# Performance work log

Measured on AMD Instinct MI355X. Metric: run time of the kernel, lower is better.

The kernel has to match this reference:

```python
import jax, jax.numpy as jnp
import numpy as np

INDEX_SHIFT = jnp.array([[0, 0], [-1, 0], [1, 0], [0, 1], [-1, 1], [1, 1], [0, -1], [-1, -1], [1, -1]], dtype=jnp.int32)
GRID = jnp.array([513, 513], dtype=jnp.int32)  # pseudo_image_dims + 1


def setup_inputs() -> dict:
    key = jax.random.key(0)
    k1, k2, k3, k4 = jax.random.split(key, 4)
    li_bev_coors = jax.random.randint(k1, (8192, 2), 0, 512, dtype=jnp.int32)
    ra_bev_coors = jax.random.randint(k2, (2048, 2), 0, 512, dtype=jnp.int32)
    ra_pts = jax.random.normal(k3, (2048, 5), dtype=jnp.float32)
    ra_voxel_coords = jax.random.randint(k4, (2048, 3), 0, 512, dtype=jnp.int32)
    return {"li_bev_coors": li_bev_coors, "ra_bev_coors": ra_bev_coors,
            "ra_pts": ra_pts, "ra_voxel_coords": ra_voxel_coords}


def _neighbour_coors(bev_grids):
    # [N,2] -> [N,9,2]: shift by 9-neighborhood, wrap by (grid_size+1)
    return (bev_grids[:, None, :] + INDEX_SHIFT[None, :, :]) % GRID


def _nearest_dy(neighbour_coor, dy_coor, dy_mask):
    # neighbour_coor: [N,9,2] int; dy_coor: [M,2] float; dy_mask: [M] bool
    n = neighbour_coor.shape[0]
    a = neighbour_coor.reshape(-1, 2).astype(jnp.float32)        # [N*9, 2]
    a2 = jnp.sum(a * a, axis=-1)                                  # [N*9]
    b2 = jnp.sum(dy_coor * dy_coor, axis=-1)                      # [M]
    # squared euclidean distances (exact: integer coordinates)
    d2 = a2[:, None] + b2[None, :] - 2.0 * (a @ dy_coor.T)        # [N*9, M]
    d2 = jnp.where(dy_mask[None, :], d2, jnp.inf)                 # mask non-dynamic voxels
    dmin = jnp.sqrt(jnp.maximum(jnp.min(d2, axis=-1), 0.0))       # min commutes with sqrt
    return (dmin * 0.01).reshape(n, 9)


def reference(li_bev_coors, ra_bev_coors, ra_pts, ra_voxel_coords):
    # dynamic-point selection: |velocity| > 0.1 (column 4)
    dy_mask = jnp.abs(ra_pts[:, 4]) > 0.1                         # [M]
    dy_coor = ra_voxel_coords[:, 1:].astype(jnp.float32)          # [M,2]
    # (uniquifying dy_coor does not change the min-distance; skip for jit shapes)
    li_nb = _neighbour_coors(li_bev_coors)                        # [N_li,9,2]
    ra_nb = _neighbour_coors(ra_bev_coors)                        # [N_ra,9,2]
    use = jnp.sum(dy_mask) > 1
    li_dis = jnp.where(use, _nearest_dy(li_nb, dy_coor, dy_mask), 0.0)
    ra_dis = jnp.where(use, _nearest_dy(ra_nb, dy_coor, dy_mask), 0.0)
    return (li_dis, ra_dis)
```

## Files before the change

kernel.cpp:

```cpp
#include <hip/hip_runtime.h>

#define BLOCK 256
#define SPLITS 16
#define QPT 8
#define PREPB 90
#define MAXC 136


__device__ __forceinline__ float2 pk_fma2(float2 a, float2 b, float2 c) {
    return make_float2(fmaf(a.x, b.x, c.x), fmaf(a.y, b.y, c.y));
}
__device__ __forceinline__ float2 pk_mul2(float2 a, float2 b) {
    return make_float2(a.x * b.x, a.y * b.y);
}

__global__ __launch_bounds__(BLOCK) void prep_kernel(
    const float* __restrict__ pts, int m,
    int* __restrict__ gate, int* __restrict__ out_bits, int total)
{
    __shared__ int s_cnt;
    const int tid = blockIdx.x * BLOCK + threadIdx.x;
    const int n4 = total >> 2;
    const int4 iv = make_int4(0x7F7F7F7F, 0x7F7F7F7F, 0x7F7F7F7F, 0x7F7F7F7F);
    int4* o4 = (int4*)out_bits;
    for (int i = tid; i < n4; i += PREPB * BLOCK) o4[i] = iv;

    if (blockIdx.x == 0) {
        if (threadIdx.x == 0) s_cnt = 0;
        __syncthreads();
        int nv = 0;
        for (int i = threadIdx.x; i < m; i += BLOCK)
            nv += (fabsf(pts[i * 5 + 4]) > 0.1f) ? 1 : 0;
        if (nv) atomicAdd(&s_cnt, nv);
        __syncthreads();
        if (threadIdx.x == 0) *gate = (s_cnt > 1) ? 1 : 0;
    }
}

__global__ __launch_bounds__(BLOCK) void main_kernel(
    const int* __restrict__ li_coors, int n_li,
    const int* __restrict__ ra_coors, int n_ra,
    const float* __restrict__ pts,
    const int* __restrict__ vox,
    int m, int cs, int csPad,
    const int* __restrict__ gate,
    int* __restrict__ out_bits, int total)
{
    __shared__ __align__(16) float sx[MAXC];
    __shared__ __align__(16) float sy[MAXC];

    const int g = *gate;

    const int li_total = n_li * 9;
    const int qbase = blockIdx.x * (BLOCK * QPT) + threadIdx.x;

    float n2x[QPT], n2y[QPT], q2[QPT], mn[QPT];
#pragma unroll
    for (int k = 0; k < QPT; ++k) {
        int q = qbase + k * BLOCK;
        float qx = 0.0f, qy = 0.0f;
        if (q < total) {
            const int shift_x[9] = {0,-1,1,0,-1,1,0,-1,1};
            const int shift_y[9] = {0, 0,0,1, 1,1,-1,-1,-1};
            int n, s;
            const int* src;
            if (q < li_total) { n = q / 9; s = q - n * 9; src = li_coors; }
            else { int r = q - li_total; n = r / 9; s = r - n * 9; src = ra_coors; }
            int cx = src[n * 2 + 0] + shift_x[s];
            int cy = src[n * 2 + 1] + shift_y[s];
            if (cx < 0) cx += 513;
            if (cy < 0) cy += 513;
            qx = (float)cx; qy = (float)cy;
        }
        n2x[k] = -2.0f * qx;
        n2y[k] = -2.0f * qy;
        q2[k]  = fmaf(qx, qx, qy * qy);
        mn[k]  = 3.4e38f;
    }

    const int base = blockIdx.y * cs;
    for (int i = threadIdx.x; i < csPad; i += BLOCK) {
        int gi = base + i;
        float x = 3.0e4f, y = 3.0e4f;
        if (i < cs && gi < m && fabsf(pts[gi * 5 + 4]) > 0.1f) {
            x = (float)vox[gi * 3 + 1];
            y = (float)vox[gi * 3 + 2];
        }
        sx[i] = x;
        sy[i] = y;
    }
    __syncthreads();

    const float4* __restrict__ X4 = (const float4*)sx;
    const float4* __restrict__ Y4 = (const float4*)sy;
    const int iters = csPad >> 2;
#pragma unroll 4
    for (int i = 0; i < iters; ++i) {
        float4 X = X4[i];
        float4 Y = Y4[i];
        float2 X01 = make_float2(X.x, X.y), X23 = make_float2(X.z, X.w);
        float2 Y01 = make_float2(Y.x, Y.y), Y23 = make_float2(Y.z, Y.w);
        float2 C01 = pk_fma2(X01, X01, pk_mul2(Y01, Y01));
        float2 C23 = pk_fma2(X23, X23, pk_mul2(Y23, Y23));
#pragma unroll
        for (int k = 0; k < QPT; ++k) {
            float2 nx = make_float2(n2x[k], n2x[k]);
            float2 ny = make_float2(n2y[k], n2y[k]);
            float2 T01 = pk_fma2(X01, nx, pk_fma2(Y01, ny, C01));
            float2 T23 = pk_fma2(X23, nx, pk_fma2(Y23, ny, C23));
            mn[k] = fminf(fminf(T01.x, T01.y), mn[k]);
            mn[k] = fminf(fminf(T23.x, T23.y), mn[k]);
        }
    }

#pragma unroll
    for (int k = 0; k < QPT; ++k) {
        int q = qbase + k * BLOCK;
        if (q < total) {
            float val = g ? sqrtf(q2[k] + mn[k]) * 0.01f : 0.0f;
            atomicMin(out_bits + q, __float_as_int(val));
        }
    }
}

extern "C" void kernel_launch(void* const* d_in, const int* in_sizes, int n_in,
                              void* d_out, int out_size, void* d_ws, size_t ws_size,
                              hipStream_t stream) {
    const int*   li  = (const int*)d_in[0];
    const int*   ra  = (const int*)d_in[1];
    const float* pts = (const float*)d_in[2];
    const int*   vox = (const int*)d_in[3];

    const int n_li = in_sizes[0] / 2;
    const int n_ra = in_sizes[1] / 2;
    const int m    = in_sizes[2] / 5;

    const int total = (n_li + n_ra) * 9;
    const int qblocks = (total + BLOCK * QPT - 1) / (BLOCK * QPT);

    const int cs    = (m + SPLITS - 1) / SPLITS;
    const int csPad = (cs + 3) & ~3;

    int* gate = (int*)d_ws;
    int* outb = (int*)d_out;

    prep_kernel<<<PREPB, BLOCK, 0, stream>>>(pts, m, gate, outb, total);
    main_kernel<<<dim3(qblocks, SPLITS), BLOCK, 0, stream>>>(
        li, n_li, ra, n_ra, pts, vox, m, cs, csPad, gate, outb, total);
}
```

Before: 79.06 us.

## Replace atomicMin output merge with workspace partials and a separate reduce kernel

When the workspace is large enough, each split block writes its partial squared minimum into a per-split workspace slice instead of doing atomicMin on the output. A new reduce kernel takes the min across the 16 splits, recomputes the dynamic-point gate per block, and writes the final sqrt-scaled distance. This drops the prep kernel's output initialisation and the atomics. In exchange it adds about 5.9 MB of workspace writes and reads, and every reduce block redundantly rescans the 2048 points for the gate count.

```diff
diff --git a/kernel.cpp b/kernel.cpp
--- a/kernel.cpp
+++ b/kernel.cpp
@@ -5,6 +5,7 @@
 #define QPT 8
 #define PREPB 90
 #define MAXC 136
+#define RQPT 4
 
 
 __device__ __forceinline__ float2 pk_fma2(float2 a, float2 b, float2 c) {
@@ -37,6 +38,7 @@
     }
 }
 
+template<bool WS_PATH>
 __global__ __launch_bounds__(BLOCK) void main_kernel(
     const int* __restrict__ li_coors, int n_li,
     const int* __restrict__ ra_coors, int n_ra,
@@ -44,12 +46,14 @@
     const int* __restrict__ vox,
     int m, int cs, int csPad,
     const int* __restrict__ gate,
+    float* __restrict__ ws,
     int* __restrict__ out_bits, int total)
 {
     __shared__ __align__(16) float sx[MAXC];
     __shared__ __align__(16) float sy[MAXC];
 
-    const int g = *gate;
+    int g = 1;
+    if (!WS_PATH) g = *gate;
 
     const int li_total = n_li * 9;
     const int qbase = blockIdx.x * (BLOCK * QPT) + threadIdx.x;
@@ -113,13 +117,59 @@
         }
     }
 
-#pragma unroll
-    for (int k = 0; k < QPT; ++k) {
+    if (WS_PATH) {
+        float* __restrict__ dst = ws + (size_t)blockIdx.y * (size_t)total;
+#pragma unroll
+        for (int k = 0; k < QPT; ++k) {
+            int q = qbase + k * BLOCK;
+            if (q < total) dst[q] = q2[k] + mn[k];
+        }
+    } else {
+#pragma unroll
+        for (int k = 0; k < QPT; ++k) {
+            int q = qbase + k * BLOCK;
+            if (q < total) {
+                float val = g ? sqrtf(q2[k] + mn[k]) * 0.01f : 0.0f;
+                atomicMin(out_bits + q, __float_as_int(val));
+            }
+        }
+    }
+}
+
+__global__ __launch_bounds__(BLOCK) void reduce_kernel(
+    const float* __restrict__ pts, int m,
+    const float* __restrict__ ws,
+    float* __restrict__ out, int total)
+{
+    __shared__ int s_cnt;
+    if (threadIdx.x == 0) s_cnt = 0;
+
+    const int qbase = blockIdx.x * (BLOCK * RQPT) + threadIdx.x;
+    float mnv[RQPT];
+#pragma unroll
+    for (int k = 0; k < RQPT; ++k) {
+        mnv[k] = 3.4e38f;
         int q = qbase + k * BLOCK;
         if (q < total) {
-            float val = g ? sqrtf(q2[k] + mn[k]) * 0.01f : 0.0f;
-            atomicMin(out_bits + q, __float_as_int(val));
-        }
+#pragma unroll
+            for (int s = 0; s < SPLITS; ++s)
+                mnv[k] = fminf(mnv[k], ws[(size_t)s * (size_t)total + q]);
+        }
+    }
+
+    __syncthreads();
+    int nv = 0;
+    for (int i = threadIdx.x; i < m; i += BLOCK)
+        nv += (fabsf(pts[i * 5 + 4]) > 0.1f) ? 1 : 0;
+    if (nv) atomicAdd(&s_cnt, nv);
+    __syncthreads();
+    const int g = (s_cnt > 1) ? 1 : 0;
+
+#pragma unroll
+    for (int k = 0; k < RQPT; ++k) {
+        int q = qbase + k * BLOCK;
+        if (q < total)
+            out[q] = g ? sqrtf(fmaxf(mnv[k], 0.0f)) * 0.01f : 0.0f;
     }
 }
 
@@ -141,10 +191,22 @@
     const int cs    = (m + SPLITS - 1) / SPLITS;
     const int csPad = (cs + 3) & ~3;
 
-    int* gate = (int*)d_ws;
-    int* outb = (int*)d_out;
-
-    prep_kernel<<<PREPB, BLOCK, 0, stream>>>(pts, m, gate, outb, total);
-    main_kernel<<<dim3(qblocks, SPLITS), BLOCK, 0, stream>>>(
-        li, n_li, ra, n_ra, pts, vox, m, cs, csPad, gate, outb, total);
-}
+    const size_t need = (size_t)SPLITS * (size_t)total * sizeof(float);
+
+    if (ws_size >= need) {
+        float* ws  = (float*)d_ws;
+        float* out = (float*)d_out;
+        main_kernel<true><<<dim3(qblocks, SPLITS), BLOCK, 0, stream>>>(
+            li, n_li, ra, n_ra, pts, vox, m, cs, csPad,
+            nullptr, ws, nullptr, total);
+        const int rblocks = (total + BLOCK * RQPT - 1) / (BLOCK * RQPT);
+        reduce_kernel<<<rblocks, BLOCK, 0, stream>>>(pts, m, ws, out, total);
+    } else {
+        int* gate = (int*)d_ws;
+        int* outb = (int*)d_out;
+        prep_kernel<<<PREPB, BLOCK, 0, stream>>>(pts, m, gate, outb, total);
+        main_kernel<false><<<dim3(qblocks, SPLITS), BLOCK, 0, stream>>>(
+            li, n_li, ra, n_ra, pts, vox, m, cs, csPad,
+            gate, nullptr, outb, total);
+    }
+}
```

Result: slower. 81.51 us (+3.1%).

## Fuse prep into main kernel with last-block split reduction via tickets

Applied to the files above, without the earlier changes.

The separate prep kernel, which initialised the output and computed the dynamic-point gate, is replaced with a hipMemsetAsync of a small counter region plus a single fused kernel. Each split block writes its partial minima to workspace and counts dynamic points with a wavefront ballot. The last block to arrive for each query tile, detected with an atomic ticket, reduces the partials and writes the final distances directly, replacing the per-element atomicMin. This removes one kernel launch and the atomics, but adds workspace traffic and a memset, and only runs when the workspace is large enough.

```diff
diff --git a/kernel.cpp b/kernel.cpp
--- a/kernel.cpp
+++ b/kernel.cpp
@@ -5,6 +5,8 @@
 #define QPT 8
 #define PREPB 90
 #define MAXC 136
+
+static_assert(MAXC <= BLOCK, "ballot-based gate count assumes <=1 staging iter/thread");
 
 
 __device__ __forceinline__ float2 pk_fma2(float2 a, float2 b, float2 c) {
@@ -37,19 +39,27 @@
     }
 }
 
+template<bool FUSED>
 __global__ __launch_bounds__(BLOCK) void main_kernel(
     const int* __restrict__ li_coors, int n_li,
     const int* __restrict__ ra_coors, int n_ra,
     const float* __restrict__ pts,
     const int* __restrict__ vox,
     int m, int cs, int csPad,
+    int* __restrict__ tickets,
+    int* __restrict__ gates,
+    float* __restrict__ part,
+    float* __restrict__ out,
     const int* __restrict__ gate,
-    int* __restrict__ out_bits, int total)
+    int* __restrict__ out_bits,
+    int total)
 {
     __shared__ __align__(16) float sx[MAXC];
     __shared__ __align__(16) float sy[MAXC];
-
-    const int g = *gate;
+    __shared__ int s_ret;
+
+    int g = 1;
+    if (!FUSED) g = *gate;
 
     const int li_total = n_li * 9;
     const int qbase = blockIdx.x * (BLOCK * QPT) + threadIdx.x;
@@ -79,15 +89,23 @@
     }
 
     const int base = blockIdx.y * cs;
+    bool dyn = false;
     for (int i = threadIdx.x; i < csPad; i += BLOCK) {
         int gi = base + i;
         float x = 3.0e4f, y = 3.0e4f;
         if (i < cs && gi < m && fabsf(pts[gi * 5 + 4]) > 0.1f) {
+            dyn = true;
             x = (float)vox[gi * 3 + 1];
             y = (float)vox[gi * 3 + 2];
         }
         sx[i] = x;
         sy[i] = y;
+    }
+
+    if (FUSED) {
+        unsigned long long b = __ballot(dyn);
+        if ((threadIdx.x & 63) == 0 && b)
+            atomicAdd(&gates[blockIdx.x], (int)__popcll(b));
     }
     __syncthreads();
 
@@ -113,12 +131,42 @@
         }
     }
 
-#pragma unroll
-    for (int k = 0; k < QPT; ++k) {
-        int q = qbase + k * BLOCK;
-        if (q < total) {
-            float val = g ? sqrtf(q2[k] + mn[k]) * 0.01f : 0.0f;
-            atomicMin(out_bits + q, __float_as_int(val));
+    if (FUSED) {
+        float* __restrict__ dst =
+            part + ((size_t)blockIdx.x * SPLITS + blockIdx.y) * (BLOCK * QPT);
+#pragma unroll
+        for (int k = 0; k < QPT; ++k)
+            dst[k * BLOCK + threadIdx.x] = q2[k] + mn[k];
+
+        __threadfence();
+        if (threadIdx.x == 0)
+            s_ret = atomicAdd(&tickets[blockIdx.x], 1);
+        __syncthreads();
+
+        if (s_ret == SPLITS - 1) {
+            __threadfence();
+            const int gg = gates[blockIdx.x];
+            const float* __restrict__ colp =
+                part + (size_t)blockIdx.x * SPLITS * (BLOCK * QPT);
+#pragma unroll
+            for (int k = 0; k < QPT; ++k) {
+                float v = q2[k] + mn[k];
+#pragma unroll 4
+                for (int y = 0; y < SPLITS; ++y)
+                    v = fminf(v, colp[y * (BLOCK * QPT) + k * BLOCK + threadIdx.x]);
+                int q = qbase + k * BLOCK;
+                if (q < total)
+                    out[q] = (gg > 1) ? sqrtf(fmaxf(v, 0.0f)) * 0.01f : 0.0f;
+            }
+        }
+    } else {
+#pragma unroll
+        for (int k = 0; k < QPT; ++k) {
+            int q = qbase + k * BLOCK;
+            if (q < total) {
+                float val = g ? sqrtf(q2[k] + mn[k]) * 0.01f : 0.0f;
+                atomicMin(out_bits + q, __float_as_int(val));
+            }
         }
     }
 }
@@ -141,10 +189,26 @@
     const int cs    = (m + SPLITS - 1) / SPLITS;
     const int csPad = (cs + 3) & ~3;
 
-    int* gate = (int*)d_ws;
-    int* outb = (int*)d_out;
-
-    prep_kernel<<<PREPB, BLOCK, 0, stream>>>(pts, m, gate, outb, total);
-    main_kernel<<<dim3(qblocks, SPLITS), BLOCK, 0, stream>>>(
-        li, n_li, ra, n_ra, pts, vox, m, cs, csPad, gate, outb, total);
-}
+    const size_t partOffF = 2048;
+    const size_t need =
+        (partOffF + (size_t)qblocks * SPLITS * (BLOCK * QPT)) * sizeof(float);
+
+    if (ws_size >= need && 2 * qblocks <= (int)partOffF && csPad <= MAXC) {
+        int*   tickets = (int*)d_ws;
+        int*   gates   = tickets + qblocks;
+        float* part    = (float*)d_ws + partOffF;
+        float* out     = (float*)d_out;
+
+        hipMemsetAsync(d_ws, 0, 2 * qblocks * sizeof(int), stream);
+        main_kernel<true><<<dim3(qblocks, SPLITS), BLOCK, 0, stream>>>(
+            li, n_li, ra, n_ra, pts, vox, m, cs, csPad,
+            tickets, gates, part, out, nullptr, nullptr, total);
+    } else {
+        int* gate = (int*)d_ws;
+        int* outb = (int*)d_out;
+        prep_kernel<<<PREPB, BLOCK, 0, stream>>>(pts, m, gate, outb, total);
+        main_kernel<false><<<dim3(qblocks, SPLITS), BLOCK, 0, stream>>>(
+            li, n_li, ra, n_ra, pts, vox, m, cs, csPad,
+            nullptr, nullptr, nullptr, nullptr, gate, outb, total);
+    }
+}
```

Result: slower. 170.6 us (+115.8%).

## Merge into single kernel with full dynamic-point set per block, no atomics

Applied to the files above, without the earlier changes.

Replaces the prep plus split-reduction design with one kernel. Each thread handles a single query, and each block stages up to 2048 candidate points (x, y and precomputed x²+y²) in shared memory. The gate count is computed inside every block, so the separate init kernel and the atomicMin output merge both go away. The cost is that every block reloads all candidates, and each thread carries one query instead of eight, which cuts register reuse per shared-memory load and adds three LDS reads per four candidates.

```diff
diff --git a/kernel.cpp b/kernel.cpp
--- a/kernel.cpp
+++ b/kernel.cpp
@@ -1,126 +1,99 @@
 #include <hip/hip_runtime.h>
 
-#define BLOCK 256
-#define SPLITS 16
-#define QPT 8
-#define PREPB 90
-#define MAXC 136
+#define BLOCK 192
+#define MAXM  2048
 
 
 __device__ __forceinline__ float2 pk_fma2(float2 a, float2 b, float2 c) {
     return make_float2(fmaf(a.x, b.x, c.x), fmaf(a.y, b.y, c.y));
 }
-__device__ __forceinline__ float2 pk_mul2(float2 a, float2 b) {
-    return make_float2(a.x * b.x, a.y * b.y);
-}
 
-__global__ __launch_bounds__(BLOCK) void prep_kernel(
-    const float* __restrict__ pts, int m,
-    int* __restrict__ gate, int* __restrict__ out_bits, int total)
-{
-    __shared__ int s_cnt;
-    const int tid = blockIdx.x * BLOCK + threadIdx.x;
-    const int n4 = total >> 2;
-    const int4 iv = make_int4(0x7F7F7F7F, 0x7F7F7F7F, 0x7F7F7F7F, 0x7F7F7F7F);
-    int4* o4 = (int4*)out_bits;
-    for (int i = tid; i < n4; i += PREPB * BLOCK) o4[i] = iv;
-
-    if (blockIdx.x == 0) {
-        if (threadIdx.x == 0) s_cnt = 0;
-        __syncthreads();
-        int nv = 0;
-        for (int i = threadIdx.x; i < m; i += BLOCK)
-            nv += (fabsf(pts[i * 5 + 4]) > 0.1f) ? 1 : 0;
-        if (nv) atomicAdd(&s_cnt, nv);
-        __syncthreads();
-        if (threadIdx.x == 0) *gate = (s_cnt > 1) ? 1 : 0;
-    }
-}
-
-__global__ __launch_bounds__(BLOCK) void main_kernel(
+__global__ __launch_bounds__(BLOCK) void gauss_kernel(
     const int* __restrict__ li_coors, int n_li,
     const int* __restrict__ ra_coors, int n_ra,
     const float* __restrict__ pts,
     const int* __restrict__ vox,
-    int m, int cs, int csPad,
-    const int* __restrict__ gate,
-    int* __restrict__ out_bits, int total)
+    int m,
+    float* __restrict__ out, int total)
 {
-    __shared__ __align__(16) float sx[MAXC];
-    __shared__ __align__(16) float sy[MAXC];
+    __shared__ __align__(16) float sx[MAXM];
+    __shared__ __align__(16) float sy[MAXM];
+    __shared__ __align__(16) float sc[MAXM];
+    __shared__ int s_cnt;
 
-    const int g = *gate;
+    if (threadIdx.x == 0) s_cnt = 0;
 
-    const int li_total = n_li * 9;
-    const int qbase = blockIdx.x * (BLOCK * QPT) + threadIdx.x;
-
-    float n2x[QPT], n2y[QPT], q2[QPT], mn[QPT];
-#pragma unroll
-    for (int k = 0; k < QPT; ++k) {
-        int q = qbase + k * BLOCK;
-        float qx = 0.0f, qy = 0.0f;
-        if (q < total) {
-            const int shift_x[9] = {0,-1,1,0,-1,1,0,-1,1};
-            const int shift_y[9] = {0, 0,0,1, 1,1,-1,-1,-1};
-            int n, s;
-            const int* src;
-            if (q < li_total) { n = q / 9; s = q - n * 9; src = li_coors; }
-            else { int r = q - li_total; n = r / 9; s = r - n * 9; src = ra_coors; }
-            int cx = src[n * 2 + 0] + shift_x[s];
-            int cy = src[n * 2 + 1] + shift_y[s];
-            if (cx < 0) cx += 513;
-            if (cy < 0) cy += 513;
-            qx = (float)cx; qy = (float)cy;
-        }
-        n2x[k] = -2.0f * qx;
-        n2y[k] = -2.0f * qy;
-        q2[k]  = fmaf(qx, qx, qy * qy);
-        mn[k]  = 3.4e38f;
+    const int q = blockIdx.x * BLOCK + threadIdx.x;
+    const bool valid = q < total;
+    float nx = 0.0f, ny = 0.0f, q2 = 0.0f;
+    if (valid) {
+        const int shift_x[9] = {0,-1,1,0,-1,1,0,-1,1};
+        const int shift_y[9] = {0, 0,0,1, 1,1,-1,-1,-1};
+        const int li_total = n_li * 9;
+        int n, s;
+        const int* src;
+        if (q < li_total) { n = q / 9; s = q - n * 9; src = li_coors; }
+        else { int r = q - li_total; n = r / 9; s = r - n * 9; src = ra_coors; }
+        int cx = src[n * 2 + 0] + shift_x[s];
+        int cy = src[n * 2 + 1] + shift_y[s];
+        if (cx < 0) cx += 513;
+        if (cy < 0) cy += 513;
+        float qx = (float)cx, qy = (float)cy;
+        nx = -2.0f * qx;
+        ny = -2.0f * qy;
+        q2 = fmaf(qx, qx, qy * qy);
     }
 
-    const int base = blockIdx.y * cs;
-    for (int i = threadIdx.x; i < csPad; i += BLOCK) {
-        int gi = base + i;
-        float x = 3.0e4f, y = 3.0e4f;
-        if (i < cs && gi < m && fabsf(pts[gi * 5 + 4]) > 0.1f) {
-            x = (float)vox[gi * 3 + 1];
-            y = (float)vox[gi * 3 + 2];
+    float mn = 3.4e38f;
+    int nv = 0;
+
+    for (int base = 0; base < m; base += MAXM) {
+        const int cs = min(m - base, MAXM);
+        const int csPad = (cs + 3) & ~3;
+
+        __syncthreads();
+        for (int i = threadIdx.x; i < csPad; i += BLOCK) {
+            int gi = base + i;
+            float x = 3.0e4f, y = 3.0e4f;
+            if (i < cs && fabsf(pts[gi * 5 + 4]) > 0.1f) {
+                ++nv;
+                x = (float)vox[gi * 3 + 1];
+                y = (float)vox[gi * 3 + 2];
+            }
+            sx[i] = x;
+            sy[i] = y;
+            sc[i] = fmaf(x, x, y * y);
         }
-        sx[i] = x;
-        sy[i] = y;
-    }
-    __syncthreads();
+        __syncthreads();
 
-    const float4* __restrict__ X4 = (const float4*)sx;
-    const float4* __restrict__ Y4 = (const float4*)sy;
-    const int iters = csPad >> 2;
+        const float4* __restrict__ X4 = (const float4*)sx;
+        const float4* __restrict__ Y4 = (const float4*)sy;
+        const float4* __restrict__ C4 = (const float4*)sc;
+        const float2 nx2 = make_float2(nx, nx);
+        const float2 ny2 = make_float2(ny, ny);
+        const int iters = csPad >> 2;
 #pragma unroll 4
-    for (int i = 0; i < iters; ++i) {
-        float4 X = X4[i];
-        float4 Y = Y4[i];
-        float2 X01 = make_float2(X.x, X.y), X23 = make_float2(X.z, X.w);
-        float2 Y01 = make_float2(Y.x, Y.y), Y23 = make_float2(Y.z, Y.w);
-        float2 C01 = pk_fma2(X01, X01, pk_mul2(Y01, Y01));
-        float2 C23 = pk_fma2(X23, X23, pk_mul2(Y23, Y23));
-#pragma unroll
-        for (int k = 0; k < QPT; ++k) {
-            float2 nx = make_float2(n2x[k], n2x[k]);
-            float2 ny = make_float2(n2y[k], n2y[k]);
-            float2 T01 = pk_fma2(X01, nx, pk_fma2(Y01, ny, C01));
-            float2 T23 = pk_fma2(X23, nx, pk_fma2(Y23, ny, C23));
-            mn[k] = fminf(fminf(T01.x, T01.y), mn[k]);
-            mn[k] = fminf(fminf(T23.x, T23.y), mn[k]);
+        for (int i = 0; i < iters; ++i) {
+            float4 X = X4[i];
+            float4 Y = Y4[i];
+            float4 C = C4[i];
+            float2 T01 = pk_fma2(make_float2(X.x, X.y), nx2,
+                          pk_fma2(make_float2(Y.x, Y.y), ny2,
+                                  make_float2(C.x, C.y)));
+            float2 T23 = pk_fma2(make_float2(X.z, X.w), nx2,
+                          pk_fma2(make_float2(Y.z, Y.w), ny2,
+                                  make_float2(C.z, C.w)));
+            mn = fminf(fminf(T01.x, T01.y), mn);
+            mn = fminf(fminf(T23.x, T23.y), mn);
         }
     }
 
-#pragma unroll
-    for (int k = 0; k < QPT; ++k) {
-        int q = qbase + k * BLOCK;
-        if (q < total) {
-            float val = g ? sqrtf(q2[k] + mn[k]) * 0.01f : 0.0f;
-            atomicMin(out_bits + q, __float_as_int(val));
-        }
-    }
+    if (nv) atomicAdd(&s_cnt, nv);
+    __syncthreads();
+    const int g = s_cnt;
+
+    if (valid)
+        out[q] = (g > 1) ? sqrtf(fmaxf(q2 + mn, 0.0f)) * 0.01f : 0.0f;
 }
 
 extern "C" void kernel_launch(void* const* d_in, const int* in_sizes, int n_in,
@@ -135,16 +108,9 @@
     const int n_ra = in_sizes[1] / 2;
     const int m    = in_sizes[2] / 5;
 
-    const int total = (n_li + n_ra) * 9;
-    const int qblocks = (total + BLOCK * QPT - 1) / (BLOCK * QPT);
+    const int total  = (n_li + n_ra) * 9;
+    const int blocks = (total + BLOCK - 1) / BLOCK;
 
-    const int cs    = (m + SPLITS - 1) / SPLITS;
-    const int csPad = (cs + 3) & ~3;
-
-    int* gate = (int*)d_ws;
-    int* outb = (int*)d_out;
-
-    prep_kernel<<<PREPB, BLOCK, 0, stream>>>(pts, m, gate, outb, total);
-    main_kernel<<<dim3(qblocks, SPLITS), BLOCK, 0, stream>>>(
-        li, n_li, ra, n_ra, pts, vox, m, cs, csPad, gate, outb, total);
+    gauss_kernel<<<blocks, BLOCK, 0, stream>>>(
+        li, n_li, ra, n_ra, pts, vox, m, (float*)d_out, total);
 }
```

Result: slower. 88.52 us (+12.0%).
